# Optimization experiments

Measured on AMD Instinct MI355X. Metric: run time of the kernel, lower is better.

## Reference

```python
import jax, jax.numpy as jnp
import numpy as np

EPS = 1e-6
V_LO, V_HI = 0.95, 1.05
N_NODES = 100000
N_EDGES = 3200000


def setup_inputs() -> dict:
    key = jax.random.key(0)
    k1, k2, k3, k4 = jax.random.split(key, 4)
    node_features = jax.random.normal(k1, (N_NODES, 4), dtype=jnp.float32)
    edge_index = jax.random.randint(k2, (2, N_EDGES), 0, N_NODES, dtype=jnp.int64)
    edge_probs = jax.random.uniform(k3, (N_EDGES,), dtype=jnp.float32)
    edge_params = jax.random.uniform(k4, (N_EDGES, 2), dtype=jnp.float32)
    return {
        "node_features": node_features,
        "edge_index": edge_index,
        "edge_probs": edge_probs,
        "edge_params": edge_params,
    }


def reference(node_features, edge_index, edge_probs, edge_params):
    n_nodes = node_features.shape[0]
    src = edge_index[0]
    dst = edge_index[1]

    # power flow on each edge, computed from the SRC node voltage magnitude
    v_mag_src = jnp.sqrt(node_features[src, 0] ** 2 + node_features[src, 1] ** 2)  # [E]
    v2 = v_mag_src ** 2
    p_e = v2 / (edge_params[:, 0] + EPS) * edge_probs  # [E]
    q_e = v2 / (edge_params[:, 1] + EPS) * edge_probs  # [E]

    # each edge contributes to both endpoints; self-loops contribute only once
    self_loop = src == dst
    p_e_dst = jnp.where(self_loop, 0.0, p_e)
    q_e_dst = jnp.where(self_loop, 0.0, q_e)

    p_flow = (jax.ops.segment_sum(p_e, src, num_segments=n_nodes)
              + jax.ops.segment_sum(p_e_dst, dst, num_segments=n_nodes))  # [N]
    q_flow = (jax.ops.segment_sum(q_e, src, num_segments=n_nodes)
              + jax.ops.segment_sum(q_e_dst, dst, num_segments=n_nodes))  # [N]

    p_load = node_features[:, 2]
    q_load = node_features[:, 3]
    power_balance_loss = jnp.mean((p_load + p_flow) ** 2 + (q_load + q_flow) ** 2)

    # voltage magnitude box constraint
    v_mag = jnp.sqrt(node_features[:, 0] ** 2 + node_features[:, 1] ** 2)
    lower_viol = jax.nn.relu(V_LO - v_mag)
    upper_viol = jax.nn.relu(v_mag - V_HI)
    voltage_loss = jnp.mean(lower_viol ** 2 + upper_viol ** 2)

    return power_balance_loss + voltage_loss
```

## Files before the change

kernel.cpp:

```cpp
#include <hip/hip_runtime.h>

#define EPS 1e-6f
#define V_LO 0.95f
#define V_HI 1.05f

#define BIN_ELEMS 20480
#define TPB 1024
#define MAX_SPLIT 51

__global__ __launch_bounds__(TPB) void pf_edge_scan(
    const float* __restrict__ nf,
    const int* __restrict__ ei,
    const float* __restrict__ probs,
    const float* __restrict__ params,
    float2* __restrict__ partial,
    int n_edges, int n_nodes, int nbins, int per_chunk)
{
    extern __shared__ float2 lds[];
    int bin  = blockIdx.x % nbins;
    int slot = blockIdx.x / nbins;
    int node_base = bin * BIN_ELEMS;

    for (int i = threadIdx.x; i < BIN_ELEMS; i += TPB)
        lds[i] = make_float2(0.0f, 0.0f);
    __syncthreads();

    int e0 = slot * per_chunk;
    int e1 = min(e0 + per_chunk, n_edges);

    for (int e = e0 + threadIdx.x * 2; e < e1; e += TPB * 2) {
        int2   s2  = *reinterpret_cast<const int2*>(&ei[e]);
        int2   d2  = *reinterpret_cast<const int2*>(&ei[n_edges + e]);
        float2 pb2 = *reinterpret_cast<const float2*>(&probs[e]);
        float4 pr2 = *reinterpret_cast<const float4*>(&params[(size_t)e * 2]);

        #pragma unroll
        for (int k = 0; k < 2; ++k) {
            int   src  = k ? s2.y : s2.x;
            int   dst  = k ? d2.y : d2.x;
            float prob = k ? pb2.y : pb2.x;
            float prx  = k ? pr2.z : pr2.x;
            float pry  = k ? pr2.w : pr2.y;

            unsigned ls = (unsigned)(src - node_base);
            unsigned ld = (unsigned)(dst - node_base);
            bool cs = ls < (unsigned)BIN_ELEMS;
            bool cd = (ld < (unsigned)BIN_ELEMS) & (src != dst);
            if (cs | cd) {
                float2 v = *reinterpret_cast<const float2*>(&nf[(size_t)src * 4]);
                float v2 = v.x * v.x + v.y * v.y;
                float pe = v2 / (prx + EPS) * prob;
                float qe = v2 / (pry + EPS) * prob;
                if (cs) {
                    atomicAdd(&lds[ls].x, pe);
                    atomicAdd(&lds[ls].y, qe);
                }
                if (cd) {
                    atomicAdd(&lds[ld].x, pe);
                    atomicAdd(&lds[ld].y, qe);
                }
            }
        }
    }
    __syncthreads();

    int lim = min(BIN_ELEMS, n_nodes - node_base);
    float2* out = partial + (size_t)slot * n_nodes + node_base;
    for (int i = threadIdx.x; i < lim; i += TPB)
        out[i] = lds[i];
}

__global__ void pf_node_kernel(const float* __restrict__ nf,
                               const float2* __restrict__ partial,
                               float* __restrict__ acc,
                               int n_nodes, int split) {
    int i = blockIdx.x * blockDim.x + threadIdx.x;
    float c = 0.0f;
    if (i < n_nodes) {
        float4 f = *reinterpret_cast<const float4*>(&nf[(size_t)i * 4]);
        float p = f.z, q = f.w;
        const float2* pp = partial + i;
        for (int s = 0; s < split; ++s) {
            float2 fl = pp[(size_t)s * n_nodes];
            p += fl.x;
            q += fl.y;
        }
        float vmag = sqrtf(f.x * f.x + f.y * f.y);
        float lv = fmaxf(V_LO - vmag, 0.0f);
        float uv = fmaxf(vmag - V_HI, 0.0f);
        c = p * p + q * q + lv * lv + uv * uv;
    }
    #pragma unroll
    for (int off = 32; off > 0; off >>= 1)
        c += __shfl_down(c, off);
    __shared__ float wsum[4];
    int lane = threadIdx.x & 63;
    int wid  = threadIdx.x >> 6;
    if (lane == 0) wsum[wid] = c;
    __syncthreads();
    if (threadIdx.x == 0) {
        float s = 0.0f;
        int nw = blockDim.x >> 6;
        for (int w = 0; w < nw; ++w) s += wsum[w];
        atomicAdd(acc, s);
    }
}

__global__ void pf_finalize_kernel(const float* __restrict__ acc,
                                   float* __restrict__ out,
                                   float inv_n) {
    out[0] = acc[0] * inv_n;
}

extern "C" void kernel_launch(void* const* d_in, const int* in_sizes, int n_in,
                              void* d_out, int out_size, void* d_ws, size_t ws_size,
                              hipStream_t stream) {
    const float* nf     = (const float*)d_in[0];
    const int*   ei     = (const int*)d_in[1];
    const float* probs  = (const float*)d_in[2];
    const float* params = (const float* )d_in[3];

    int n_nodes = in_sizes[0] / 4;
    int n_edges = in_sizes[2];

    float*  acc     = (float*)d_ws;
    float2* partial = (float2*)((char*)d_ws + 256);

    size_t slot_bytes = (size_t)n_nodes * sizeof(float2);
    int split = (int)((ws_size - 256) / slot_bytes);
    if (split > MAX_SPLIT) split = MAX_SPLIT;
    if (split < 1) split = 1;

    int nbins = (n_nodes + BIN_ELEMS - 1) / BIN_ELEMS;
    int per_chunk = (n_edges + split - 1) / split;
    per_chunk = (per_chunk + 1) & ~1;

    size_t lds_bytes = (size_t)BIN_ELEMS * sizeof(float2);
    hipFuncSetAttribute((const void*)pf_edge_scan,
                        hipFuncAttributeMaxDynamicSharedMemorySize,
                        (int)lds_bytes);

    hipMemsetAsync(d_ws, 0, 256, stream);

    pf_edge_scan<<<nbins * split, TPB, lds_bytes, stream>>>(
        nf, ei, probs, params, partial, n_edges, n_nodes, nbins, per_chunk);

    int nblocks = (n_nodes + 255) / 256;
    pf_node_kernel<<<nblocks, 256, 0, stream>>>(nf, partial, acc, n_nodes, split);

    pf_finalize_kernel<<<1, 1, 0, stream>>>(acc, (float*)d_out,
                                            1.0f / (float)n_nodes);
}
```

Before: 112.3 us.

## Precompute per-node v2 table, widen edge batch to 4, use fast reciprocal

Adds a small pre-pass that computes each node's squared voltage magnitude into a compact table. The edge scan then gathers one float per source instead of a float2 from a 16-byte-strided row. The edge loop now handles 4 edges per thread with 128-bit loads and issues all gathers up front to expose more memory parallelism, and it replaces the divisions with hardware reciprocal approximations. Partial outputs use nontemporal stores and loads. The cost is an extra kernel launch, a tail path, and slightly lower precision from rcp.

```diff
diff --git a/kernel.cpp b/kernel.cpp
--- a/kernel.cpp
+++ b/kernel.cpp
@@ -7,57 +7,92 @@
 #define BIN_ELEMS 20480
 #define TPB 1024
 #define MAX_SPLIT 51
+#define BATCH 4
+
+typedef float f32x2 __attribute__((ext_vector_type(2)));
+
+__global__ void pf_v2_kernel(const float4* __restrict__ nf4,
+                             float* __restrict__ v2tab, int n_nodes) {
+    int i = blockIdx.x * blockDim.x + threadIdx.x;
+    if (i < n_nodes) {
+        float4 f = nf4[i];
+        v2tab[i] = f.x * f.x + f.y * f.y;
+    }
+}
 
 __global__ __launch_bounds__(TPB) void pf_edge_scan(
-    const float* __restrict__ nf,
+    const float* __restrict__ v2tab,
     const int* __restrict__ ei,
     const float* __restrict__ probs,
     const float* __restrict__ params,
-    float2* __restrict__ partial,
+    float* __restrict__ partial,
     int n_edges, int n_nodes, int nbins, int per_chunk)
 {
-    extern __shared__ float2 lds[];
+    extern __shared__ float lds[];
     int bin  = blockIdx.x % nbins;
     int slot = blockIdx.x / nbins;
     int node_base = bin * BIN_ELEMS;
 
-    for (int i = threadIdx.x; i < BIN_ELEMS; i += TPB)
-        lds[i] = make_float2(0.0f, 0.0f);
+    for (int i = threadIdx.x; i < 2 * BIN_ELEMS; i += TPB)
+        lds[i] = 0.0f;
     __syncthreads();
 
     int e0 = slot * per_chunk;
     int e1 = min(e0 + per_chunk, n_edges);
 
-    for (int e = e0 + threadIdx.x * 2; e < e1; e += TPB * 2) {
-        int2   s2  = *reinterpret_cast<const int2*>(&ei[e]);
-        int2   d2  = *reinterpret_cast<const int2*>(&ei[n_edges + e]);
-        float2 pb2 = *reinterpret_cast<const float2*>(&probs[e]);
-        float4 pr2 = *reinterpret_cast<const float4*>(&params[(size_t)e * 2]);
+    for (int e = e0 + threadIdx.x * BATCH; e < e1; e += TPB * BATCH) {
+        if (e + BATCH <= e1) {
+            int4   s4  = *reinterpret_cast<const int4*>(&ei[e]);
+            int4   d4  = *reinterpret_cast<const int4*>(&ei[n_edges + e]);
+            float4 pb4 = *reinterpret_cast<const float4*>(&probs[e]);
+            float4 prA = *reinterpret_cast<const float4*>(&params[(size_t)e * 2]);
+            float4 prB = *reinterpret_cast<const float4*>(&params[(size_t)e * 2 + 4]);
 
-        #pragma unroll
-        for (int k = 0; k < 2; ++k) {
-            int   src  = k ? s2.y : s2.x;
-            int   dst  = k ? d2.y : d2.x;
-            float prob = k ? pb2.y : pb2.x;
-            float prx  = k ? pr2.z : pr2.x;
-            float pry  = k ? pr2.w : pr2.y;
+            float v2_0 = v2tab[s4.x];
+            float v2_1 = v2tab[s4.y];
+            float v2_2 = v2tab[s4.z];
+            float v2_3 = v2tab[s4.w];
 
-            unsigned ls = (unsigned)(src - node_base);
-            unsigned ld = (unsigned)(dst - node_base);
-            bool cs = ls < (unsigned)BIN_ELEMS;
-            bool cd = (ld < (unsigned)BIN_ELEMS) & (src != dst);
-            if (cs | cd) {
-                float2 v = *reinterpret_cast<const float2*>(&nf[(size_t)src * 4]);
-                float v2 = v.x * v.x + v.y * v.y;
-                float pe = v2 / (prx + EPS) * prob;
-                float qe = v2 / (pry + EPS) * prob;
-                if (cs) {
-                    atomicAdd(&lds[ls].x, pe);
-                    atomicAdd(&lds[ls].y, qe);
+            #pragma unroll
+            for (int k = 0; k < BATCH; ++k) {
+                int   src  = (k == 0) ? s4.x : (k == 1) ? s4.y : (k == 2) ? s4.z : s4.w;
+                int   dst  = (k == 0) ? d4.x : (k == 1) ? d4.y : (k == 2) ? d4.z : d4.w;
+                float prob = (k == 0) ? pb4.x : (k == 1) ? pb4.y : (k == 2) ? pb4.z : pb4.w;
+                float prx  = (k == 0) ? prA.x : (k == 1) ? prA.z : (k == 2) ? prB.x : prB.z;
+                float pry  = (k == 0) ? prA.y : (k == 1) ? prA.w : (k == 2) ? prB.y : prB.w;
+                float v2   = (k == 0) ? v2_0 : (k == 1) ? v2_1 : (k == 2) ? v2_2 : v2_3;
+
+                unsigned ls = (unsigned)(src - node_base);
+                unsigned ld = (unsigned)(dst - node_base);
+                bool cs = ls < (unsigned)BIN_ELEMS;
+                bool cd = (ld < (unsigned)BIN_ELEMS) & (src != dst);
+                if (cs | cd) {
+                    float pe = v2 * prob * __builtin_amdgcn_rcpf(prx + EPS);
+                    float qe = v2 * prob * __builtin_amdgcn_rcpf(pry + EPS);
+                    if (cs) {
+                        atomicAdd(&lds[2 * ls],     pe);
+                        atomicAdd(&lds[2 * ls + 1], qe);
+                    }
+                    if (cd) {
+                        atomicAdd(&lds[2 * ld],     pe);
+                        atomicAdd(&lds[2 * ld + 1], qe);
+                    }
                 }
-                if (cd) {
-                    atomicAdd(&lds[ld].x, pe);
-                    atomicAdd(&lds[ld].y, qe);
+            }
+        } else {
+            for (int t = e; t < e1; ++t) {
+                int src = ei[t];
+                int dst = ei[n_edges + t];
+                unsigned ls = (unsigned)(src - node_base);
+                unsigned ld = (unsigned)(dst - node_base);
+                bool cs = ls < (unsigned)BIN_ELEMS;
+                bool cd = (ld < (unsigned)BIN_ELEMS) & (src != dst);
+                if (cs | cd) {
+                    float v2 = v2tab[src];
+                    float pe = v2 * probs[t] * __builtin_amdgcn_rcpf(params[(size_t)t * 2] + EPS);
+                    float qe = v2 * probs[t] * __builtin_amdgcn_rcpf(params[(size_t)t * 2 + 1] + EPS);
+                    if (cs) { atomicAdd(&lds[2 * ls], pe); atomicAdd(&lds[2 * ls + 1], qe); }
+                    if (cd) { atomicAdd(&lds[2 * ld], pe); atomicAdd(&lds[2 * ld + 1], qe); }
                 }
             }
         }
@@ -65,13 +100,15 @@
     __syncthreads();
 
     int lim = min(BIN_ELEMS, n_nodes - node_base);
-    float2* out = partial + (size_t)slot * n_nodes + node_base;
+    float* out = partial + (size_t)slot * n_nodes * 2 + (size_t)node_base * 2;
+    const f32x2* lds2 = reinterpret_cast<const f32x2*>(lds);
+    f32x2* out2 = reinterpret_cast<f32x2*>(out);
     for (int i = threadIdx.x; i < lim; i += TPB)
-        out[i] = lds[i];
+        __builtin_nontemporal_store(lds2[i], &out2[i]);
 }
 
 __global__ void pf_node_kernel(const float* __restrict__ nf,
-                               const float2* __restrict__ partial,
+                               const float* __restrict__ partial,
                                float* __restrict__ acc,
                                int n_nodes, int split) {
     int i = blockIdx.x * blockDim.x + threadIdx.x;
@@ -79,9 +116,9 @@
     if (i < n_nodes) {
         float4 f = *reinterpret_cast<const float4*>(&nf[(size_t)i * 4]);
         float p = f.z, q = f.w;
-        const float2* pp = partial + i;
+        const f32x2* pp = reinterpret_cast<const f32x2*>(partial) + i;
         for (int s = 0; s < split; ++s) {
-            float2 fl = pp[(size_t)s * n_nodes];
+            f32x2 fl = __builtin_nontemporal_load(&pp[(size_t)s * n_nodes]);
             p += fl.x;
             q += fl.y;
         }
@@ -118,32 +155,37 @@
     const float* nf     = (const float*)d_in[0];
     const int*   ei     = (const int*)d_in[1];
     const float* probs  = (const float*)d_in[2];
-    const float* params = (const float* )d_in[3];
+    const float* params = (const float*)d_in[3];
 
     int n_nodes = in_sizes[0] / 4;
     int n_edges = in_sizes[2];
 
-    float*  acc     = (float*)d_ws;
-    float2* partial = (float2*)((char*)d_ws + 256);
+    float* acc   = (float*)d_ws;
+    float* v2tab = (float*)((char*)d_ws + 256);
+    size_t v2_bytes = ((size_t)n_nodes * sizeof(float) + 255) & ~(size_t)255;
+    float* partial = (float*)((char*)d_ws + 256 + v2_bytes);
 
-    size_t slot_bytes = (size_t)n_nodes * sizeof(float2);
-    int split = (int)((ws_size - 256) / slot_bytes);
+    size_t slot_bytes = (size_t)n_nodes * 2 * sizeof(float);
+    int split = (int)((ws_size - 256 - v2_bytes) / slot_bytes);
     if (split > MAX_SPLIT) split = MAX_SPLIT;
     if (split < 1) split = 1;
 
     int nbins = (n_nodes + BIN_ELEMS - 1) / BIN_ELEMS;
     int per_chunk = (n_edges + split - 1) / split;
-    per_chunk = (per_chunk + 1) & ~1;
+    per_chunk = (per_chunk + 3) & ~3;
 
-    size_t lds_bytes = (size_t)BIN_ELEMS * sizeof(float2);
-    hipFuncSetAttribute((const void*)pf_edge_scan,
-                        hipFuncAttributeMaxDynamicSharedMemorySize,
-                        (int)lds_bytes);
+    size_t lds_bytes = (size_t)(2 * BIN_ELEMS) * sizeof(float);
+    (void)hipFuncSetAttribute((const void*)pf_edge_scan,
+                              hipFuncAttributeMaxDynamicSharedMemorySize,
+                              (int)lds_bytes);
 
-    hipMemsetAsync(d_ws, 0, 256, stream);
+    (void)hipMemsetAsync(d_ws, 0, 256, stream);
+
+    pf_v2_kernel<<<(n_nodes + 255) / 256, 256, 0, stream>>>(
+        (const float4*)nf, v2tab, n_nodes);
 
     pf_edge_scan<<<nbins * split, TPB, lds_bytes, stream>>>(
-        nf, ei, probs, params, partial, n_edges, n_nodes, nbins, per_chunk);
+        v2tab, ei, probs, params, partial, n_edges, n_nodes, nbins, per_chunk);
 
     int nblocks = (n_nodes + 255) / 256;
     pf_node_kernel<<<nblocks, 256, 0, stream>>>(nf, partial, acc, n_nodes, split);
```

New measurement: 124.8 us. +11.2%, slower.
